# Kernel optimization log

Hardware: AMD Instinct MI355X
Metric: run time of the kernel (lower is better)

The kernel has to match this reference:

```python
import jax, jax.numpy as jnp
import numpy as np
from jax import lax

# Straight-through sign: forward sign(x), backward passes grad where |x|<=1 (hardtanh STE)
@jax.custom_vjp
def sign_ste(x):
    return jnp.sign(x)

def _sign_fwd(x):
    return jnp.sign(x), x

def _sign_bwd(x, g):
    return (g * (jnp.abs(x) <= 1.0).astype(g.dtype),)

sign_ste.defvjp(_sign_fwd, _sign_bwd)

STRIDE = 1
PADDING = 1

def setup_inputs() -> dict:
    key = jax.random.key(0)
    k1, k2, k3 = jax.random.split(key, 3)
    B, Cin, H, W = 32, 256, 56, 56
    Cout, K = 256, 3
    inp = jax.random.normal(k1, (B, Cin, H, W), dtype=jnp.float32)
    # kaiming-uniform-ish init like torch Conv2d default
    fan_in = Cin * K * K
    bound = 1.0 / np.sqrt(fan_in)
    weight1 = jax.random.uniform(k2, (Cout, Cin, K, K), minval=-bound, maxval=bound, dtype=jnp.float32)
    weight2 = jax.random.uniform(k3, (Cout, Cin, K, K), minval=-bound, maxval=bound, dtype=jnp.float32)
    return {"input": inp, "weight1": weight1, "weight2": weight2}

def reference(input, weight1, weight2):
    # ternarized weight: (sign(w1)+sign(w2))/2 in {-1,-0.5,0,0.5,1}
    w_ter = (sign_ste(weight1) + sign_ste(weight2)) * 0.5
    x_bin = sign_ste(input)
    out = lax.conv_general_dilated(
        x_bin, w_ter,
        window_strides=(STRIDE, STRIDE),
        padding=[(PADDING, PADDING), (PADDING, PADDING)],
        dimension_numbers=("NCHW", "OIHW", "NCHW"),
    )
    # per-output-channel scaling: mean|w1| + mean|w2| over (in, kh, kw)
    alpha = jnp.mean(jnp.abs(weight1), axis=(1, 2, 3)) + jnp.mean(jnp.abs(weight2), axis=(1, 2, 3))
    return out * alpha[None, :, None, None]
```

## Files before the change

### kernel.cpp

```cpp
#include <hip/hip_runtime.h>
#include <hip/hip_bf16.h>

#define B_    32
#define C_    256
#define H_    56
#define W_    56
#define HP    58
#define WPAD  58
#define HW    3136
#define CHW   802816
#define M_TOT 100352

typedef char  charx16 __attribute__((ext_vector_type(16)));
typedef int   intx4   __attribute__((ext_vector_type(4)));

#define XPAD_BYTES (B_ * HP * WPAD * C_)
#define WPK_BYTES  (C_ * 9 * C_)

__device__ __forceinline__ int sgn8(float f) {
  return ((f > 0.f) ? 1 : ((f < 0.f) ? -1 : 0)) & 0xff;
}

__global__ __launch_bounds__(256) void pack_w_kernel(const float* __restrict__ w1,
                                                     const float* __restrict__ w2,
                                                     char* __restrict__ wq,
                                                     float* __restrict__ alphah) {
  __shared__ float l1[2304], l2[2304];
  const int co = blockIdx.x;
  const int tid = threadIdx.x;
  const float* s1 = w1 + co * 2304;
  const float* s2 = w2 + co * 2304;
#pragma unroll
  for (int i = 0; i < 9; ++i) {
    l1[i * 256 + tid] = s1[i * 256 + tid];
    l2[i * 256 + tid] = s2[i * 256 + tid];
  }
  __syncthreads();
  const int ci = tid;
  float sabs = 0.f;
#pragma unroll
  for (int s = 0; s < 9; ++s) {
    const float a = l1[ci * 9 + s];
    const float b = l2[ci * 9 + s];
    const int sa = (a > 0.f) - (a < 0.f);
    const int sb = (b > 0.f) - (b < 0.f);
    wq[(co * 9 + s) * C_ + ci] = (char)(sa + sb);
    sabs += fabsf(a) + fabsf(b);
  }
#pragma unroll
  for (int off = 32; off > 0; off >>= 1) sabs += __shfl_down(sabs, off, 64);
  __shared__ float red[4];
  if ((tid & 63) == 0) red[tid >> 6] = sabs;
  __syncthreads();
  if (tid == 0)
    alphah[co] = (red[0] + red[1] + red[2] + red[3]) * (0.5f / 2304.0f);
}

#define ROWPC 272
__global__ __launch_bounds__(256) void pack_x_kernel(const float* __restrict__ in,
                                                     char* __restrict__ xp) {
  __shared__ char row[58 * ROWPC];
  const int yp = blockIdx.x % HP;
  const int b  = blockIdx.x / HP;
  const int tid = threadIdx.x;

  float4* rz = (float4*)row;
  const float4 z4 = make_float4(0.f, 0.f, 0.f, 0.f);
#pragma unroll
  for (int i = 0; i < 4; ++i) {
    const int idx = i * 256 + tid;
    if (idx < (58 * ROWPC) / 16) rz[idx] = z4;
  }
  __syncthreads();

  const int y = yp - 1;
  const int xq = tid % 14;
  const int cs = tid / 14;
  if (y >= 0 && y < H_ && cs < 18) {
    const float* base = in + ((size_t)b * C_ * H_ + (size_t)y) * W_ + xq * 4;
#pragma unroll
    for (int k = 0; k < 4; ++k) {
      const int cq = cs + 18 * k;
      if (cq < 64) {
        float4 f[4];
#pragma unroll
        for (int j = 0; j < 4; ++j)
          f[j] = *(const float4*)(base + (size_t)(cq * 4 + j) * (H_ * W_));
#pragma unroll
        for (int d = 0; d < 4; ++d) {
          const float v0 = (d == 0) ? f[0].x : (d == 1) ? f[0].y : (d == 2) ? f[0].z : f[0].w;
          const float v1 = (d == 0) ? f[1].x : (d == 1) ? f[1].y : (d == 2) ? f[1].z : f[1].w;
          const float v2 = (d == 0) ? f[2].x : (d == 1) ? f[2].y : (d == 2) ? f[2].z : f[2].w;
          const float v3 = (d == 0) ? f[3].x : (d == 1) ? f[3].y : (d == 2) ? f[3].z : f[3].w;
          const unsigned int pk = (unsigned)sgn8(v0) | ((unsigned)sgn8(v1) << 8) |
                                  ((unsigned)sgn8(v2) << 16) | ((unsigned)sgn8(v3) << 24);
          *(unsigned int*)&row[(xq * 4 + d + 1) * ROWPC + cq * 4] = pk;
        }
      }
    }
  }
  __syncthreads();

  const int cc = tid & 15;
  const int xo = tid >> 4;
  char* dst = xp + (size_t)(b * HP + yp) * WPAD * C_;
#pragma unroll
  for (int it = 0; it < 4; ++it) {
    const int xs = it * 16 + xo;
    if (xs < WPAD)
      *(float4*)(dst + xs * C_ + cc * 16) = *(const float4*)&row[xs * ROWPC + cc * 16];
  }
}

__global__ __launch_bounds__(256, 2) void gemm_kernel(const char* __restrict__ xp,
                                                      const char* __restrict__ wq,
                                                      const float* __restrict__ alphah,
                                                      float* __restrict__ out) {
  __shared__ char sA[2 * 128 * 128];
  __shared__ char sB[2 * 128 * 128];
  const int tid = threadIdx.x;

  const int id = blockIdx.x;
  const int xcd = id & 7;
  const int l = id >> 3;
  const int co0 = (l & 1) * 128;
  const int m0 = ((l >> 1) * 8 + xcd) * 128;

  const int srow = tid >> 3;
  const int scol = (tid & 7) ^ (srow & 7);

  const char* wsrc[4];
  const char* xsrc[4];
#pragma unroll
  for (int i = 0; i < 4; ++i) {
    const int m = m0 + srow + 32 * i;
    const int b = m / HW;
    const int rem = m - b * HW;
    const int y = rem / W_;
    const int x = rem - y * W_;
    xsrc[i] = xp + ((b * HP + y) * WPAD + x) * C_ + scol * 16;
    wsrc[i] = wq + (co0 + srow + 32 * i) * 9 * C_ + scol * 16;
  }

  intx4 acc[4][4] = {};

  const int lane = tid & 63;
  const int wave = tid >> 6;
  const int wm = wave >> 1;
  const int wn = wave & 1;
  const int lrow = lane & 15;
  const int quad = lane >> 4;
  const int swk = lrow & 7;
  const int abase = (wm * 64 + lrow) * 128;
  const int bbase = (wn * 64 + lrow) * 128;

  auto stage = [&](int t) {
    const int s = t >> 1;
    const int hh = (t & 1) * 128;
    const int woff = s * C_ + hh;
    const int shoff = ((s / 3) * WPAD + (s % 3)) * C_ + hh;
    char* dA = sA + (t & 1) * 16384 + tid * 16;
    char* dB = sB + (t & 1) * 16384 + tid * 16;
#pragma unroll
    for (int i = 0; i < 4; ++i)
      __builtin_amdgcn_global_load_lds(
          (const __attribute__((address_space(1))) void*)(wsrc[i] + woff),
          (__attribute__((address_space(3))) void*)(dA + i * 4096), 16, 0, 0);
#pragma unroll
    for (int i = 0; i < 4; ++i)
      __builtin_amdgcn_global_load_lds(
          (const __attribute__((address_space(1))) void*)(xsrc[i] + shoff),
          (__attribute__((address_space(3))) void*)(dB + i * 4096), 16, 0, 0);
  };

  stage(0);
  for (int t = 0; t < 18; ++t) {
    __syncthreads();
    if (t < 17) stage(t + 1);
    const char* bA = sA + (t & 1) * 16384;
    const char* bB = sB + (t & 1) * 16384;
#pragma unroll
    for (int kf = 0; kf < 2; ++kf) {
      const int coff = (((kf << 2) + quad) ^ swk) << 4;
      intx4 af[4], bfv[4];
#pragma unroll
      for (int i = 0; i < 4; ++i)
        af[i] = *(const intx4*)(bA + abase + i * 2048 + coff);
#pragma unroll
      for (int j = 0; j < 4; ++j)
        bfv[j] = *(const intx4*)(bB + bbase + j * 2048 + coff);
#pragma unroll
      for (int i = 0; i < 4; ++i)
#pragma unroll
        for (int j = 0; j < 4; ++j)
          acc[i][j] = __builtin_amdgcn_mfma_i32_16x16x64_i8(af[i], bfv[j],
                                                            acc[i][j], 0, 0, 0);
    }
  }

  int ob[4];
#pragma unroll
  for (int j = 0; j < 4; ++j) {
    const int m = m0 + wn * 64 + j * 16 + lrow;
    const int b = m / HW;
    const int rem = m - b * HW;
    const int y = rem / W_;
    const int x = rem - y * W_;
    ob[j] = b * CHW + y * W_ + x;
  }
#pragma unroll
  for (int i = 0; i < 4; ++i) {
#pragma unroll
    for (int r = 0; r < 4; ++r) {
      const int co = co0 + wm * 64 + i * 16 + quad * 4 + r;
      const float sc = alphah[co];
#pragma unroll
      for (int j = 0; j < 4; ++j)
        out[ob[j] + co * HW] = (float)acc[i][j][r] * sc;
    }
  }
}

extern "C" void kernel_launch(void* const* d_in, const int* in_sizes, int n_in,
                              void* d_out, int out_size, void* d_ws, size_t ws_size,
                              hipStream_t stream) {
  const float* input = (const float*)d_in[0];
  const float* w1 = (const float*)d_in[1];
  const float* w2 = (const float*)d_in[2];
  float* out = (float*)d_out;

  char* ws = (char*)d_ws;
  char* xp = ws;
  char* wq = ws + XPAD_BYTES;
  float* alphah = (float*)(ws + XPAD_BYTES + WPK_BYTES);

  pack_w_kernel<<<C_, 256, 0, stream>>>(w1, w2, wq, alphah);
  pack_x_kernel<<<B_ * HP, 256, 0, stream>>>(input, xp);
  gemm_kernel<<<M_TOT / 128 * (C_ / 128), 256, 0, stream>>>(xp, wq, alphah, out);
}
```

Measured before the change: 249.3 us.

## Enlarge GEMM tile to 128x256 with 512 threads and triple-buffered LDS pipeline

Blocks of the int8 implicit-GEMM kernel grow to 512 threads (8 waves) and cover 256 output pixels by 128 output channels. The LDS pipeline moves from double to triple buffering, with a prefetch distance of two stages, and relies on explicit vmcnt waits plus a raw s_barrier instead of __syncthreads. MFMA sections are wrapped in s_setprio. The goal is to hide global-to-LDS latency and to raise weight-tile reuse, at the cost of 144KB of LDS per block, which may limit occupancy to one block per CU.

```diff
diff --git a/kernel.cpp b/kernel.cpp
--- a/kernel.cpp
+++ b/kernel.cpp
@@ -112,73 +112,86 @@
   }
 }
 
-__global__ __launch_bounds__(256, 2) void gemm_kernel(const char* __restrict__ xp,
+#define GLL16(src, dst)                                                        \
+  __builtin_amdgcn_global_load_lds(                                            \
+      (const __attribute__((address_space(1))) void*)(src),                    \
+      (__attribute__((address_space(3))) void*)(dst), 16, 0, 0)
+
+__global__ __launch_bounds__(512, 2) void gemm_kernel(const char* __restrict__ xp,
                                                       const char* __restrict__ wq,
                                                       const float* __restrict__ alphah,
                                                       float* __restrict__ out) {
-  __shared__ char sA[2 * 128 * 128];
-  __shared__ char sB[2 * 128 * 128];
+  __shared__ char sA[3 * 128 * 128];
+  __shared__ char sB[3 * 256 * 128];
   const int tid = threadIdx.x;
 
   const int id = blockIdx.x;
   const int xcd = id & 7;
   const int l = id >> 3;
   const int co0 = (l & 1) * 128;
-  const int m0 = ((l >> 1) * 8 + xcd) * 128;
+  const int m0 = ((l >> 1) * 8 + xcd) * 256;
 
   const int srow = tid >> 3;
   const int scol = (tid & 7) ^ (srow & 7);
 
-  const char* wsrc[4];
+  const char* wsrc[2];
   const char* xsrc[4];
 #pragma unroll
+  for (int i = 0; i < 2; ++i)
+    wsrc[i] = wq + (co0 + srow + 64 * i) * 9 * C_ + scol * 16;
+#pragma unroll
   for (int i = 0; i < 4; ++i) {
-    const int m = m0 + srow + 32 * i;
+    const int m = m0 + srow + 64 * i;
     const int b = m / HW;
     const int rem = m - b * HW;
     const int y = rem / W_;
     const int x = rem - y * W_;
     xsrc[i] = xp + ((b * HP + y) * WPAD + x) * C_ + scol * 16;
-    wsrc[i] = wq + (co0 + srow + 32 * i) * 9 * C_ + scol * 16;
   }
 
   intx4 acc[4][4] = {};
 
   const int lane = tid & 63;
   const int wave = tid >> 6;
-  const int wm = wave >> 1;
-  const int wn = wave & 1;
+  const int wm = wave >> 2;
+  const int wn = wave & 3;
   const int lrow = lane & 15;
   const int quad = lane >> 4;
   const int swk = lrow & 7;
   const int abase = (wm * 64 + lrow) * 128;
   const int bbase = (wn * 64 + lrow) * 128;
 
-  auto stage = [&](int t) {
+  auto stage = [&](int t, int bufi) {
     const int s = t >> 1;
     const int hh = (t & 1) * 128;
     const int woff = s * C_ + hh;
     const int shoff = ((s / 3) * WPAD + (s % 3)) * C_ + hh;
-    char* dA = sA + (t & 1) * 16384 + tid * 16;
-    char* dB = sB + (t & 1) * 16384 + tid * 16;
+    char* dA = sA + bufi * 16384 + tid * 16;
+    char* dB = sB + bufi * 32768 + tid * 16;
+#pragma unroll
+    for (int i = 0; i < 2; ++i)
+      GLL16(wsrc[i] + woff, dA + i * 8192);
 #pragma unroll
     for (int i = 0; i < 4; ++i)
-      __builtin_amdgcn_global_load_lds(
-          (const __attribute__((address_space(1))) void*)(wsrc[i] + woff),
-          (__attribute__((address_space(3))) void*)(dA + i * 4096), 16, 0, 0);
-#pragma unroll
-    for (int i = 0; i < 4; ++i)
-      __builtin_amdgcn_global_load_lds(
-          (const __attribute__((address_space(1))) void*)(xsrc[i] + shoff),
-          (__attribute__((address_space(3))) void*)(dB + i * 4096), 16, 0, 0);
+      GLL16(xsrc[i] + shoff, dB + i * 8192);
   };
 
-  stage(0);
+  stage(0, 0);
+  asm volatile("" ::: "memory");
+  stage(1, 1);
+
+  int cb = 0;
+  int cs = 2;
   for (int t = 0; t < 18; ++t) {
-    __syncthreads();
-    if (t < 17) stage(t + 1);
-    const char* bA = sA + (t & 1) * 16384;
-    const char* bB = sB + (t & 1) * 16384;
+    if (t < 17)
+      asm volatile("s_waitcnt vmcnt(6) lgkmcnt(0)" ::: "memory");
+    else
+      asm volatile("s_waitcnt vmcnt(0) lgkmcnt(0)" ::: "memory");
+    __builtin_amdgcn_s_barrier();
+    if (t < 16) stage(t + 2, cs);
+
+    const char* bA = sA + cb * 16384;
+    const char* bB = sB + cb * 32768;
 #pragma unroll
     for (int kf = 0; kf < 2; ++kf) {
       const int coff = (((kf << 2) + quad) ^ swk) << 4;
@@ -189,13 +202,17 @@
 #pragma unroll
       for (int j = 0; j < 4; ++j)
         bfv[j] = *(const intx4*)(bB + bbase + j * 2048 + coff);
+      __builtin_amdgcn_s_setprio(1);
 #pragma unroll
       for (int i = 0; i < 4; ++i)
 #pragma unroll
         for (int j = 0; j < 4; ++j)
           acc[i][j] = __builtin_amdgcn_mfma_i32_16x16x64_i8(af[i], bfv[j],
                                                             acc[i][j], 0, 0, 0);
+      __builtin_amdgcn_s_setprio(0);
     }
+    cb = (cb == 2) ? 0 : cb + 1;
+    cs = (cs == 2) ? 0 : cs + 1;
   }
 
   int ob[4];
@@ -236,5 +253,5 @@
 
   pack_w_kernel<<<C_, 256, 0, stream>>>(w1, w2, wq, alphah);
   pack_x_kernel<<<B_ * HP, 256, 0, stream>>>(input, xp);
-  gemm_kernel<<<M_TOT / 128 * (C_ / 128), 256, 0, stream>>>(xp, wq, alphah, out);
-}
+  gemm_kernel<<<(M_TOT / 256) * (C_ / 128), 512, 0, stream>>>(xp, wq, alphah, out);
+}
```

Result: slower. 283.6 us (+13.8%).

## Merge weight and input pack kernels; stagger GEMM block start; keep k-loop rolled

Applied to the files above, without the earlier changes.

Folds the weight-packing and input-packing kernels into one launch by branching on block index, removing a kernel launch and the gap between the two. Each GEMM block also sleeps for a pseudo-random 0-3 short intervals at start to spread out the initial memory bursts, and the main k-loop is forced to stay rolled. The sleep adds a small fixed delay per block, and keeping the loop rolled can change instruction scheduling.

```diff
diff --git a/kernel.cpp b/kernel.cpp
--- a/kernel.cpp
+++ b/kernel.cpp
@@ -11,8 +11,7 @@
 #define CHW   802816
 #define M_TOT 100352
 
-typedef char  charx16 __attribute__((ext_vector_type(16)));
-typedef int   intx4   __attribute__((ext_vector_type(4)));
+typedef int intx4 __attribute__((ext_vector_type(4)));
 
 #define XPAD_BYTES (B_ * HP * WPAD * C_)
 #define WPK_BYTES  (C_ * 9 * C_)
@@ -21,96 +20,104 @@
   return ((f > 0.f) ? 1 : ((f < 0.f) ? -1 : 0)) & 0xff;
 }
 
-__global__ __launch_bounds__(256) void pack_w_kernel(const float* __restrict__ w1,
-                                                     const float* __restrict__ w2,
-                                                     char* __restrict__ wq,
-                                                     float* __restrict__ alphah) {
-  __shared__ float l1[2304], l2[2304];
-  const int co = blockIdx.x;
+#define ROWPC 272
+__global__ __launch_bounds__(256) void pack_kernel(const float* __restrict__ in,
+                                                   const float* __restrict__ w1,
+                                                   const float* __restrict__ w2,
+                                                   char* __restrict__ xp,
+                                                   char* __restrict__ wq,
+                                                   float* __restrict__ alphah) {
+  __shared__ char smem[18448];
   const int tid = threadIdx.x;
-  const float* s1 = w1 + co * 2304;
-  const float* s2 = w2 + co * 2304;
-#pragma unroll
-  for (int i = 0; i < 9; ++i) {
-    l1[i * 256 + tid] = s1[i * 256 + tid];
-    l2[i * 256 + tid] = s2[i * 256 + tid];
-  }
-  __syncthreads();
-  const int ci = tid;
-  float sabs = 0.f;
-#pragma unroll
-  for (int s = 0; s < 9; ++s) {
-    const float a = l1[ci * 9 + s];
-    const float b = l2[ci * 9 + s];
-    const int sa = (a > 0.f) - (a < 0.f);
-    const int sb = (b > 0.f) - (b < 0.f);
-    wq[(co * 9 + s) * C_ + ci] = (char)(sa + sb);
-    sabs += fabsf(a) + fabsf(b);
-  }
-#pragma unroll
-  for (int off = 32; off > 0; off >>= 1) sabs += __shfl_down(sabs, off, 64);
-  __shared__ float red[4];
-  if ((tid & 63) == 0) red[tid >> 6] = sabs;
-  __syncthreads();
-  if (tid == 0)
-    alphah[co] = (red[0] + red[1] + red[2] + red[3]) * (0.5f / 2304.0f);
-}
-
-#define ROWPC 272
-__global__ __launch_bounds__(256) void pack_x_kernel(const float* __restrict__ in,
-                                                     char* __restrict__ xp) {
-  __shared__ char row[58 * ROWPC];
-  const int yp = blockIdx.x % HP;
-  const int b  = blockIdx.x / HP;
-  const int tid = threadIdx.x;
-
-  float4* rz = (float4*)row;
-  const float4 z4 = make_float4(0.f, 0.f, 0.f, 0.f);
-#pragma unroll
-  for (int i = 0; i < 4; ++i) {
-    const int idx = i * 256 + tid;
-    if (idx < (58 * ROWPC) / 16) rz[idx] = z4;
-  }
-  __syncthreads();
-
-  const int y = yp - 1;
-  const int xq = tid % 14;
-  const int cs = tid / 14;
-  if (y >= 0 && y < H_ && cs < 18) {
-    const float* base = in + ((size_t)b * C_ * H_ + (size_t)y) * W_ + xq * 4;
-#pragma unroll
-    for (int k = 0; k < 4; ++k) {
-      const int cq = cs + 18 * k;
-      if (cq < 64) {
-        float4 f[4];
-#pragma unroll
-        for (int j = 0; j < 4; ++j)
-          f[j] = *(const float4*)(base + (size_t)(cq * 4 + j) * (H_ * W_));
-#pragma unroll
-        for (int d = 0; d < 4; ++d) {
-          const float v0 = (d == 0) ? f[0].x : (d == 1) ? f[0].y : (d == 2) ? f[0].z : f[0].w;
-          const float v1 = (d == 0) ? f[1].x : (d == 1) ? f[1].y : (d == 2) ? f[1].z : f[1].w;
-          const float v2 = (d == 0) ? f[2].x : (d == 1) ? f[2].y : (d == 2) ? f[2].z : f[2].w;
-          const float v3 = (d == 0) ? f[3].x : (d == 1) ? f[3].y : (d == 2) ? f[3].z : f[3].w;
-          const unsigned int pk = (unsigned)sgn8(v0) | ((unsigned)sgn8(v1) << 8) |
-                                  ((unsigned)sgn8(v2) << 16) | ((unsigned)sgn8(v3) << 24);
-          *(unsigned int*)&row[(xq * 4 + d + 1) * ROWPC + cq * 4] = pk;
+
+  if (blockIdx.x < B_ * HP) {
+    char* row = smem;
+    const int yp = blockIdx.x % HP;
+    const int b  = blockIdx.x / HP;
+
+    float4* rz = (float4*)row;
+    const float4 z4 = make_float4(0.f, 0.f, 0.f, 0.f);
+#pragma unroll
+    for (int i = 0; i < 4; ++i) {
+      const int idx = i * 256 + tid;
+      if (idx < (58 * ROWPC) / 16) rz[idx] = z4;
+    }
+    __syncthreads();
+
+    const int y = yp - 1;
+    const int xq = tid % 14;
+    const int cs = tid / 14;
+    if (y >= 0 && y < H_ && cs < 18) {
+      const float* base = in + ((size_t)b * C_ * H_ + (size_t)y) * W_ + xq * 4;
+#pragma unroll
+      for (int k = 0; k < 4; ++k) {
+        const int cq = cs + 18 * k;
+        if (cq < 64) {
+          float4 f[4];
+#pragma unroll
+          for (int j = 0; j < 4; ++j)
+            f[j] = *(const float4*)(base + (size_t)(cq * 4 + j) * (H_ * W_));
+#pragma unroll
+          for (int d = 0; d < 4; ++d) {
+            const float v0 = (d == 0) ? f[0].x : (d == 1) ? f[0].y : (d == 2) ? f[0].z : f[0].w;
+            const float v1 = (d == 0) ? f[1].x : (d == 1) ? f[1].y : (d == 2) ? f[1].z : f[1].w;
+            const float v2 = (d == 0) ? f[2].x : (d == 1) ? f[2].y : (d == 2) ? f[2].z : f[2].w;
+            const float v3 = (d == 0) ? f[3].x : (d == 1) ? f[3].y : (d == 2) ? f[3].z : f[3].w;
+            const unsigned int pk = (unsigned)sgn8(v0) | ((unsigned)sgn8(v1) << 8) |
+                                    ((unsigned)sgn8(v2) << 16) | ((unsigned)sgn8(v3) << 24);
+            *(unsigned int*)&row[(xq * 4 + d + 1) * ROWPC + cq * 4] = pk;
+          }
         }
       }
     }
-  }
-  __syncthreads();
-
-  const int cc = tid & 15;
-  const int xo = tid >> 4;
-  char* dst = xp + (size_t)(b * HP + yp) * WPAD * C_;
-#pragma unroll
-  for (int it = 0; it < 4; ++it) {
-    const int xs = it * 16 + xo;
-    if (xs < WPAD)
-      *(float4*)(dst + xs * C_ + cc * 16) = *(const float4*)&row[xs * ROWPC + cc * 16];
-  }
-}
+    __syncthreads();
+
+    const int cc = tid & 15;
+    const int xo = tid >> 4;
+    char* dst = xp + (size_t)(b * HP + yp) * WPAD * C_;
+#pragma unroll
+    for (int it = 0; it < 4; ++it) {
+      const int xs = it * 16 + xo;
+      if (xs < WPAD)
+        *(float4*)(dst + xs * C_ + cc * 16) = *(const float4*)&row[xs * ROWPC + cc * 16];
+    }
+  } else {
+    float* l1 = (float*)smem;
+    float* l2 = l1 + 2304;
+    float* red = (float*)(smem + 18432);
+    const int co = blockIdx.x - B_ * HP;
+    const float* s1 = w1 + co * 2304;
+    const float* s2 = w2 + co * 2304;
+#pragma unroll
+    for (int i = 0; i < 9; ++i) {
+      l1[i * 256 + tid] = s1[i * 256 + tid];
+      l2[i * 256 + tid] = s2[i * 256 + tid];
+    }
+    __syncthreads();
+    const int ci = tid;
+    float sabs = 0.f;
+#pragma unroll
+    for (int s = 0; s < 9; ++s) {
+      const float a = l1[ci * 9 + s];
+      const float b = l2[ci * 9 + s];
+      const int sa = (a > 0.f) - (a < 0.f);
+      const int sb = (b > 0.f) - (b < 0.f);
+      wq[(co * 9 + s) * C_ + ci] = (char)(sa + sb);
+      sabs += fabsf(a) + fabsf(b);
+    }
+#pragma unroll
+    for (int off = 32; off > 0; off >>= 1) sabs += __shfl_down(sabs, off, 64);
+    if ((tid & 63) == 0) red[tid >> 6] = sabs;
+    __syncthreads();
+    if (tid == 0)
+      alphah[co] = (red[0] + red[1] + red[2] + red[3]) * (0.5f / 2304.0f);
+  }
+}
+
+#define GLL16(src, dst)                                                        \
+  __builtin_amdgcn_global_load_lds(                                            \
+      (const __attribute__((address_space(1))) void*)(src),                    \
+      (__attribute__((address_space(3))) void*)(dst), 16, 0, 0)
 
 __global__ __launch_bounds__(256, 2) void gemm_kernel(const char* __restrict__ xp,
                                                       const char* __restrict__ wq,
@@ -121,6 +128,12 @@
   const int tid = threadIdx.x;
 
   const int id = blockIdx.x;
+
+  {
+    const int ph = (id ^ (id >> 3) ^ (id >> 6) ^ (id >> 9)) & 3;
+    for (int i = 0; i < ph; ++i) __builtin_amdgcn_s_sleep(8);
+  }
+
   const int xcd = id & 7;
   const int l = id >> 3;
   const int co0 = (l & 1) * 128;
@@ -163,17 +176,14 @@
     char* dB = sB + (t & 1) * 16384 + tid * 16;
 #pragma unroll
     for (int i = 0; i < 4; ++i)
-      __builtin_amdgcn_global_load_lds(
-          (const __attribute__((address_space(1))) void*)(wsrc[i] + woff),
-          (__attribute__((address_space(3))) void*)(dA + i * 4096), 16, 0, 0);
+      GLL16(wsrc[i] + woff, dA + i * 4096);
 #pragma unroll
     for (int i = 0; i < 4; ++i)
-      __builtin_amdgcn_global_load_lds(
-          (const __attribute__((address_space(1))) void*)(xsrc[i] + shoff),
-          (__attribute__((address_space(3))) void*)(dB + i * 4096), 16, 0, 0);
+      GLL16(xsrc[i] + shoff, dB + i * 4096);
   };
 
   stage(0);
+#pragma unroll 1
   for (int t = 0; t < 18; ++t) {
     __syncthreads();
     if (t < 17) stage(t + 1);
@@ -234,7 +244,6 @@
   char* wq = ws + XPAD_BYTES;
   float* alphah = (float*)(ws + XPAD_BYTES + WPK_BYTES);
 
-  pack_w_kernel<<<C_, 256, 0, stream>>>(w1, w2, wq, alphah);
-  pack_x_kernel<<<B_ * HP, 256, 0, stream>>>(input, xp);
+  pack_kernel<<<B_ * HP + C_, 256, 0, stream>>>(input, w1, w2, xp, wq, alphah);
   gemm_kernel<<<M_TOT / 128 * (C_ / 128), 256, 0, stream>>>(xp, wq, alphah, out);
 }
```

After: 261.3 us. +4.8%, slower.
